# Performance work log

Measured on AMD Instinct MI355X. Metric: run time of the kernel, lower is better.

The kernel has to match this reference:

```python
import jax, jax.numpy as jnp
import numpy as np

B, L, D, H, FD, NL, NV, NN, MAXSPD = 2, 1024, 1024, 16, 512, 4, 5000, 5000, 30
DF = 4 * D
S = L + 2  # 1 graph token + 1 sos token + L data tokens
DH = D // H
NEG = -1e9  # finite stand-in for -inf query mask (constant per softmax row -> same probs, no NaNs)


def rmsnorm(x, w, eps=1e-6):
    return x * jax.lax.rsqrt(jnp.mean(x * x, axis=-1, keepdims=True) + eps) * w


def setup_inputs() -> dict:
    key = jax.random.key(0)
    ks = jax.random.split(key, 24)
    f = lambda k, sh, s=0.02: (jax.random.normal(k, sh, jnp.float32) * s)
    return {
        "graph_features": jax.random.normal(ks[0], (B, 1, D), jnp.float32),
        "input_features": jax.random.normal(ks[1], (B, L, FD), jnp.float32),
        "proj_W": f(ks[2], (FD, D)),
        "proj_b": jnp.zeros((D,), jnp.float32),
        "sos_token": f(ks[3], (1, 1, D)),
        "node_emb": f(ks[4], (NN, D)),
        "type_emb": f(ks[5], (2, D)),
        "pos_emb": f(ks[6], (S, D)),
        "spd_emb": f(ks[7], (MAXSPD + 2, H)),
        "attn_norm_w": jnp.ones((NL, D), jnp.float32),
        "wq": f(ks[8], (NL, D, D)),
        "wk": f(ks[9], (NL, D, D)),
        "wv": f(ks[10], (NL, D, D)),
        "wo": f(ks[11], (NL, D, D)),
        "ffn_norm_w": jnp.ones((NL, D), jnp.float32),
        "w1": f(ks[12], (NL, D, DF)),
        "w2": f(ks[13], (NL, DF, D)),
        "w3": f(ks[14], (NL, D, DF)),
        "final_norm_w": jnp.ones((D,), jnp.float32),
        "out_W": f(ks[15], (D, NV)),
        "out_b": jnp.zeros((NV,), jnp.float32),
        "subnode_ids": jax.random.randint(ks[16], (B, L), 0, NN),
        "token_mask_len": jax.random.randint(ks[17], (B,), 1, L),
        "spd_indices": jax.random.randint(ks[18], (B, L, L), 0, MAXSPD + 1),
        "start_pos": 0,
    }


def reference(graph_features, input_features, proj_W, proj_b, sos_token, node_emb,
              type_emb, pos_emb, spd_emb, attn_norm_w, wq, wk, wv, wo, ffn_norm_w,
              w1, w2, w3, final_norm_w, out_W, out_b,
              subnode_ids, token_mask_len, spd_indices, start_pos):
    bsz = input_features.shape[0]
    glen = graph_features.shape[1]  # 1

    # token embedding fusion
    h_data = input_features @ proj_W + proj_b                      # [B,L,D]
    sos = jnp.broadcast_to(sos_token, (bsz, 1, D))
    h_tokens = jnp.concatenate([sos, h_data], axis=1)              # [B,L+1,D]
    sub_ext = jnp.concatenate([jnp.zeros((bsz, 1), subnode_ids.dtype), subnode_ids], axis=1)
    h_tokens = h_tokens + node_emb[sub_ext] + type_emb[0]
    h_graph = graph_features + type_emb[1]
    h = jnp.concatenate([h_graph, h_tokens], axis=1)               # [B,S,D]
    seqlen = h.shape[1]

    # SPD relative bias -> [B,H,S,S]
    max_spd = spd_emb.shape[0] - 2
    full_spd = jnp.full((bsz, seqlen, seqlen), max_spd + 1, dtype=jnp.int32)
    full_spd = full_spd.at[:, 2:, 2:].set(spd_indices.astype(jnp.int32))
    full_spd = full_spd.at[:, 0, 0].set(0).at[:, 1, 1].set(0)
    graph_bias = jnp.transpose(spd_emb[full_spd], (0, 3, 1, 2))

    h = h + pos_emb[:seqlen]

    # additive query-validity mask [B,1,S,1] broadcast over keys
    positions = jnp.arange(seqlen)[None, :]
    valid = positions < (token_mask_len[:, None] + 1 + glen)
    mask = jnp.where(valid, 0.0, NEG).astype(h.dtype)[:, None, :, None]

    scale = 1.0 / np.sqrt(DH)
    n_heads = graph_bias.shape[1]
    for i in range(wq.shape[0]):
        x = rmsnorm(h, attn_norm_w[i])
        q = (x @ wq[i]).reshape(bsz, seqlen, n_heads, DH)
        k = (x @ wk[i]).reshape(bsz, seqlen, n_heads, DH)
        v = (x @ wv[i]).reshape(bsz, seqlen, n_heads, DH)
        scores = jnp.einsum('bqhd,bkhd->bhqk', q, k) * scale + graph_bias + mask
        p = jax.nn.softmax(scores, axis=-1)
        att = jnp.einsum('bhqk,bkhd->bqhd', p, v).reshape(bsz, seqlen, D) @ wo[i]
        h = h + att
        x2 = rmsnorm(h, ffn_norm_w[i])
        h = h + (jax.nn.silu(x2 @ w1[i]) * (x2 @ w3[i])) @ w2[i]

    h = rmsnorm(h, final_norm_w)
    h_seq = h[:, glen:, :]                                          # [B,L+1,D]
    return (h_seq @ out_W + out_b).astype(jnp.float32)
```

## Files before the change

kernel.cpp:

```cpp
#include <hip/hip_runtime.h>

#define DMODEL 1024
#define DFF    4096
#define NHEAD  16
#define DHEAD  64
#define LTOK   1024
#define SEQ    1026
#define SPAD   1088
#define MPAD   2176
#define NVOC   5000
#define NVOCP  5120
#define MOUT   2050

typedef float  floatx4 __attribute__((ext_vector_type(4)));
typedef __bf16 bf16x8  __attribute__((ext_vector_type(8)));

__device__ __forceinline__ unsigned short f2b(float f) {
  unsigned int u = __builtin_bit_cast(unsigned int, f);
  u += 0x7FFFu + ((u >> 16) & 1u);
  return (unsigned short)(u >> 16);
}
__device__ __forceinline__ float b2f(unsigned short v) {
  return __builtin_bit_cast(float, ((unsigned int)v) << 16);
}
__device__ __forceinline__ void gl2lds16(const void* g, void* l) {
  __builtin_amdgcn_global_load_lds((const __attribute__((address_space(1))) void*)g,
                                   (__attribute__((address_space(3))) void*)l, 16, 0, 0);
}
__device__ __forceinline__ floatx4 mfma16(bf16x8 a, bf16x8 b, floatx4 c) {
  return __builtin_amdgcn_mfma_f32_16x16x32_bf16(a, b, c, 0, 0, 0);
}

__global__ __launch_bounds__(256) void f2b_kernel(const float* __restrict__ s,
                                                  unsigned short* __restrict__ d, int n) {
  int i = (blockIdx.x * 256 + threadIdx.x) * 4;
  if (i >= n) return;
  float4 v = *(const float4*)(s + i);
  ushort4 o; o.x = f2b(v.x); o.y = f2b(v.y); o.z = f2b(v.z); o.w = f2b(v.w);
  *(ushort4*)(d + i) = o;
}

__global__ __launch_bounds__(256) void transconv_kernel(
    const float* __restrict__ p0, const float* __restrict__ p1,
    const float* __restrict__ p2, const float* __restrict__ p3,
    unsigned short* __restrict__ dst, long dstZ, int R, int C) {
  const float* src = (blockIdx.z == 0) ? p0 : (blockIdx.z == 1) ? p1 : (blockIdx.z == 2) ? p2 : p3;
  dst += dstZ * blockIdx.z;
  __shared__ float T[64][68];
  const int r0 = blockIdx.y * 64, c0 = blockIdx.x * 64;
  const int tr = threadIdx.x >> 4, tc = threadIdx.x & 15;
#pragma unroll
  for (int it = 0; it < 4; it++) {
    int rl = tr + it * 16;
    int cg = c0 + tc * 4;
    float4 v = {0.f, 0.f, 0.f, 0.f};
    if (cg < C) v = *(const float4*)(src + (size_t)(r0 + rl) * C + cg);
    T[rl][tc * 4 + 0] = v.x; T[rl][tc * 4 + 1] = v.y;
    T[rl][tc * 4 + 2] = v.z; T[rl][tc * 4 + 3] = v.w;
  }
  __syncthreads();
#pragma unroll
  for (int it = 0; it < 4; it++) {
    int ol = tr + it * 16;
    int oc = c0 + ol;
    if (oc < C) {
      ushort4 o;
      o.x = f2b(T[tc * 4 + 0][ol]); o.y = f2b(T[tc * 4 + 1][ol]);
      o.z = f2b(T[tc * 4 + 2][ol]); o.w = f2b(T[tc * 4 + 3][ol]);
      *(ushort4*)(dst + (size_t)oc * R + r0 + tc * 4) = o;
    }
  }
}

__global__ __launch_bounds__(256) void build_h_kernel(
    float* __restrict__ h, const float* __restrict__ gf, const float* __restrict__ sos,
    const float* __restrict__ nodeE, const float* __restrict__ typeE,
    const float* __restrict__ posE, const int* __restrict__ sub) {
  const int s = blockIdx.x, b = blockIdx.y;
  const int c = threadIdx.x * 4;
  float* o = h + ((size_t)(b * SPAD + s)) * DMODEL + c;
  if (s >= SEQ) { o[0] = 0.f; o[1] = 0.f; o[2] = 0.f; o[3] = 0.f; return; }
  float4 p = *(const float4*)(posE + (size_t)s * DMODEL + c);
  if (s == 0) {
    float4 g = *(const float4*)(gf + (size_t)b * DMODEL + c);
    float4 t = *(const float4*)(typeE + DMODEL + c);
    o[0] = g.x + t.x + p.x; o[1] = g.y + t.y + p.y;
    o[2] = g.z + t.z + p.z; o[3] = g.w + t.w + p.w;
  } else {
    float4 t = *(const float4*)(typeE + c);
    int nid = (s == 1) ? 0 : sub[b * LTOK + s - 2];
    float4 ne = *(const float4*)(nodeE + (size_t)nid * DMODEL + c);
    if (s == 1) {
      float4 ss = *(const float4*)(sos + c);
      o[0] = ss.x + ne.x + t.x + p.x; o[1] = ss.y + ne.y + t.y + p.y;
      o[2] = ss.z + ne.z + t.z + p.z; o[3] = ss.w + ne.w + t.w + p.w;
    } else {
      o[0] += ne.x + t.x + p.x; o[1] += ne.y + t.y + p.y;
      o[2] += ne.z + t.z + p.z; o[3] += ne.w + t.w + p.w;
    }
  }
}

__global__ __launch_bounds__(256) void rmsnorm_kernel(const float* __restrict__ h,
                                                      const float* __restrict__ w,
                                                      unsigned short* __restrict__ out,
                                                      int final_mode) {
  const int r = blockIdx.x;
  int srow = r;
  if (final_mode) {
    if (r >= MOUT) {
      ushort4 z = {0, 0, 0, 0};
      *(ushort4*)(out + (size_t)r * DMODEL + threadIdx.x * 4) = z;
      return;
    }
    int b = r / 1025;
    srow = b * SPAD + 1 + (r - b * 1025);
  }
  float4 x = *(const float4*)(h + (size_t)srow * DMODEL + threadIdx.x * 4);
  float ss = x.x * x.x + x.y * x.y + x.z * x.z + x.w * x.w;
#pragma unroll
  for (int off = 32; off > 0; off >>= 1) ss += __shfl_down(ss, off);
  __shared__ float red[4];
  if ((threadIdx.x & 63) == 0) red[threadIdx.x >> 6] = ss;
  __syncthreads();
  float rs = rsqrtf((red[0] + red[1] + red[2] + red[3]) * (1.f / 1024.f) + 1e-6f);
  float4 ww = *(const float4*)(w + threadIdx.x * 4);
  ushort4 o;
  o.x = f2b(x.x * rs * ww.x); o.y = f2b(x.y * rs * ww.y);
  o.z = f2b(x.z * rs * ww.z); o.w = f2b(x.w * rs * ww.w);
  *(ushort4*)(out + (size_t)r * DMODEL + threadIdx.x * 4) = o;
}

__global__ __launch_bounds__(320) void bidx_kernel(const int* __restrict__ spd,
                                                   unsigned char* __restrict__ bidx) {
  const int qg = blockIdx.x, b = blockIdx.y;
  const int i0 = threadIdx.x * 4;
  if (i0 >= SPAD) return;
  const int g = i0 >> 6, c = (i0 >> 2) & 15;
  unsigned char v[4];
#pragma unroll
  for (int n = 0; n < 4; n++) {
    int kg = g * 64 + n * 16 + c;
    unsigned char vv;
    if (qg >= SEQ || kg >= SEQ) {
      vv = 32;
    } else if (qg >= 2 && kg >= 2) {
      int idx = spd[((size_t)b * LTOK + (qg - 2)) * LTOK + (kg - 2)];
      vv = (unsigned char)(idx < 0 ? 0 : (idx > 31 ? 31 : idx));
    } else {
      vv = (qg == kg) ? 0 : 31;
    }
    v[n] = vv;
  }
  uchar4 o; o.x = v[0]; o.y = v[1]; o.z = v[2]; o.w = v[3];
  *(uchar4*)(bidx + ((size_t)b * SPAD + qg) * SPAD + i0) = o;
}

__global__ __launch_bounds__(256) void vtrans_kernel(const unsigned short* __restrict__ v,
                                                     unsigned short* __restrict__ vt) {
  const int st = blockIdx.x, hh = blockIdx.y, b = blockIdx.z;
  __shared__ unsigned short T[64][72];
  const int tr = threadIdx.x >> 4, tc = threadIdx.x & 15;
#pragma unroll
  for (int it = 0; it < 4; it++) {
    int r = tr + it * 16;
    ushort4 val = *(const ushort4*)(v + ((size_t)(b * SPAD + st * 64 + r)) * DMODEL + hh * DHEAD + tc * 4);
    T[r][tc * 4 + 0] = val.x; T[r][tc * 4 + 1] = val.y;
    T[r][tc * 4 + 2] = val.z; T[r][tc * 4 + 3] = val.w;
  }
  __syncthreads();
#pragma unroll
  for (int it = 0; it < 4; it++) {
    int d = tr + it * 16;
    ushort4 o;
    o.x = T[tc * 4 + 0][d]; o.y = T[tc * 4 + 1][d];
    o.z = T[tc * 4 + 2][d]; o.w = T[tc * 4 + 3][d];
    *(ushort4*)(vt + (((size_t)(b * NHEAD + hh)) * DHEAD + d) * SPAD + st * 64 + tc * 4) = o;
  }
}

#define PST 80
__global__ __launch_bounds__(512) void attn_kernel(
    const unsigned short* __restrict__ qb, const unsigned short* __restrict__ kb,
    const unsigned short* __restrict__ vt, unsigned short* __restrict__ attb,
    const float* __restrict__ spdE, const unsigned char* __restrict__ bidx,
    const int* __restrict__ tml) {
  const int hb = blockIdx.x;
  const int qt = blockIdx.y;
  const int hh = hb >> 1, bb = hb & 1;
  const int tid = threadIdx.x;
  const int w = tid >> 6, lane = tid & 63;
  const int quad = lane >> 4, l16 = lane & 15;

  __shared__ unsigned short Qs[128 * PST];
  __shared__ unsigned short Ks[64 * PST];
  __shared__ unsigned short Vts[64 * PST];
  __shared__ unsigned short Ps[8 * 16 * PST];
  __shared__ unsigned char Is[128 * 64];
  __shared__ float bias_tab[33];

  if (tid < 33) bias_tab[tid] = (tid < 32) ? spdE[tid * NHEAD + hh] : -3.0e38f;

#pragma unroll
  for (int jj = 0; jj < 2; jj++) {
    int c = tid + (jj << 9);
    int r = c >> 3, ch = c & 7;
    int qrow = qt * 128 + r; qrow = qrow < SPAD ? qrow : SPAD - 1;
    int4 val = *(const int4*)(qb + ((size_t)(bb * SPAD + qrow)) * DMODEL + hh * DHEAD + ch * 8);
    *(int4*)(Qs + r * PST + ch * 8) = val;
  }
  const int tmlb = tml[bb];

  const int sr = tid >> 3, sch = tid & 7;
  const int ir = tid >> 2, ic = (tid & 3) * 16;
  const int irow = min(qt * 128 + ir, SPAD - 1);
  int4 kreg, vreg, ireg;
  kreg = *(const int4*)(kb + ((size_t)(bb * SPAD + sr)) * DMODEL + hh * DHEAD + sch * 8);
  vreg = *(const int4*)(vt + (((size_t)(bb * NHEAD + hh)) * DHEAD + sr) * SPAD + sch * 8);
  ireg = *(const int4*)(bidx + ((size_t)bb * SPAD + irow) * SPAD + ic);
  __syncthreads();

  bf16x8 aq[2];
  aq[0] = *(const bf16x8*)(Qs + (w * 16 + l16) * PST + quad * 8);
  aq[1] = *(const bf16x8*)(Qs + (w * 16 + l16) * PST + 32 + quad * 8);

  floatx4 O[4];
  float m_i[4], l_i[4];
#pragma unroll
  for (int d = 0; d < 4; d++) { floatx4 z = {0.f, 0.f, 0.f, 0.f}; O[d] = z; }
#pragma unroll
  for (int r = 0; r < 4; r++) { m_i[r] = -3.0e38f; l_i[r] = 0.f; }

  unsigned short* PsW = Ps + w * 16 * PST;
  float maskv[4];
#pragma unroll
  for (int r = 0; r < 4; r++) {
    int qg = qt * 128 + w * 16 + quad * 4 + r;
    maskv[r] = (qg < tmlb + 2) ? 0.f : -1.0e9f;
  }

  for (int kt = 0; kt < 17; kt++) {
    *(int4*)(Ks + sr * PST + sch * 8) = kreg;
    *(int4*)(Vts + sr * PST + sch * 8) = vreg;
    *(int4*)(Is + ir * 64 + ic) = ireg;
    __syncthreads();

    if (kt < 16) {
      const int kn = kt + 1;
      kreg = *(const int4*)(kb + ((size_t)(bb * SPAD + kn * 64 + sr)) * DMODEL + hh * DHEAD + sch * 8);
      vreg = *(const int4*)(vt + (((size_t)(bb * NHEAD + hh)) * DHEAD + sr) * SPAD + kn * 64 + sch * 8);
      ireg = *(const int4*)(bidx + ((size_t)bb * SPAD + irow) * SPAD + kn * 64 + ic);
    }

    float sc[4][4];
#pragma unroll
    for (int ns = 0; ns < 4; ns++) {
      bf16x8 bk0 = *(const bf16x8*)(Ks + (ns * 16 + l16) * PST + quad * 8);
      bf16x8 bk1 = *(const bf16x8*)(Ks + (ns * 16 + l16) * PST + 32 + quad * 8);
      floatx4 c4 = {0.f, 0.f, 0.f, 0.f};
      c4 = mfma16(aq[0], bk0, c4);
      c4 = mfma16(aq[1], bk1, c4);
#pragma unroll
      for (int r = 0; r < 4; r++) sc[ns][r] = c4[r];
    }

#pragma unroll
    for (int r = 0; r < 4; r++) {
      int row = w * 16 + quad * 4 + r;
      unsigned int iw = *(const unsigned int*)(Is + row * 64 + l16 * 4);
#pragma unroll
      for (int ns = 0; ns < 4; ns++) {
        int idx = (iw >> (8 * ns)) & 0xff;
        sc[ns][r] = sc[ns][r] * 0.125f + bias_tab[idx] + maskv[r];
      }
    }

    float alpha[4];
#pragma unroll
    for (int r = 0; r < 4; r++) {
      float mx = fmaxf(fmaxf(sc[0][r], sc[1][r]), fmaxf(sc[2][r], sc[3][r]));
#pragma unroll
      for (int off = 1; off < 16; off <<= 1) mx = fmaxf(mx, __shfl_xor(mx, off));
      float mn = fmaxf(m_i[r], mx);
      alpha[r] = __expf(m_i[r] - mn);
      m_i[r] = mn;
      float rs = 0.f;
#pragma unroll
      for (int ns = 0; ns < 4; ns++) { float p = __expf(sc[ns][r] - mn); sc[ns][r] = p; rs += p; }
#pragma unroll
      for (int off = 1; off < 16; off <<= 1) rs += __shfl_xor(rs, off);
      l_i[r] = l_i[r] * alpha[r] + rs;
    }

#pragma unroll
    for (int ns = 0; ns < 4; ns++)
#pragma unroll
      for (int r = 0; r < 4; r++)
        PsW[(quad * 4 + r) * PST + ns * 16 + l16] = f2b(sc[ns][r]);

#pragma unroll
    for (int d = 0; d < 4; d++)
#pragma unroll
      for (int r = 0; r < 4; r++) O[d][r] *= alpha[r];

    bf16x8 ap0 = *(const bf16x8*)(PsW + l16 * PST + quad * 8);
    bf16x8 ap1 = *(const bf16x8*)(PsW + l16 * PST + 32 + quad * 8);
#pragma unroll
    for (int d = 0; d < 4; d++) {
      bf16x8 bv0 = *(const bf16x8*)(Vts + (d * 16 + l16) * PST + quad * 8);
      bf16x8 bv1 = *(const bf16x8*)(Vts + (d * 16 + l16) * PST + 32 + quad * 8);
      O[d] = mfma16(ap0, bv0, O[d]);
      O[d] = mfma16(ap1, bv1, O[d]);
    }
    __syncthreads();
  }

#pragma unroll
  for (int r = 0; r < 4; r++) {
    int qg = qt * 128 + w * 16 + quad * 4 + r;
    if (qg < SPAD) {
      float inv = 1.0f / l_i[r];
#pragma unroll
      for (int d = 0; d < 4; d++)
        attb[((size_t)(bb * SPAD + qg)) * DMODEL + hh * DHEAD + d * 16 + l16] = f2b(O[d][r] * inv);
    }
  }
}

__global__ __launch_bounds__(256) void silumul_kernel(const unsigned short* __restrict__ u,
                                                      unsigned short* __restrict__ g, int n) {
  int i = (blockIdx.x * 256 + threadIdx.x) * 4;
  if (i >= n) return;
  const unsigned short* u3 = u + n;
  ushort4 a = *(const ushort4*)(u + i);
  ushort4 c = *(const ushort4*)(u3 + i);
  ushort4 o;
  float x, y;
  x = b2f(a.x); y = b2f(c.x); o.x = f2b(x / (1.f + __expf(-x)) * y);
  x = b2f(a.y); y = b2f(c.y); o.y = f2b(x / (1.f + __expf(-x)) * y);
  x = b2f(a.z); y = b2f(c.z); o.z = f2b(x / (1.f + __expf(-x)) * y);
  x = b2f(a.w); y = b2f(c.w); o.w = f2b(x / (1.f + __expf(-x)) * y);
  *(ushort4*)(g + i) = o;
}

enum { EPI_BF16 = 0, EPI_RESID = 1, EPI_PROJ = 2, EPI_OUT = 3, EPI_ATOMIC = 4 };

template <int EPI>
__global__ __launch_bounds__(256) void gemm_bt_kernel(
    const unsigned short* __restrict__ A, const unsigned short* __restrict__ Bt,
    void* __restrict__ Cv, const float* __restrict__ bias,
    int M, int N, int K, int ld, long zA, long zB, long zC, int Mreal, int Nreal) {
  A += zA * blockIdx.z;
  Bt += zB * blockIdx.z;
  char* Cb = (char*)Cv + zC * blockIdx.z;

  const int tid = threadIdx.x;
  const int lane = tid & 63, wave = tid >> 6;
  const int quad = lane >> 4, l16 = lane & 15;
  const int wr = wave >> 1, wc = wave & 1;
  const int m0 = blockIdx.y << 7, n0 = blockIdx.x << 7;

  __shared__ unsigned short As[128 * 32];
  __shared__ unsigned short Bs[128 * 32];

  floatx4 acc[4][4];
  {
    floatx4 z = {0.f, 0.f, 0.f, 0.f};
#pragma unroll
    for (int i = 0; i < 4; i++)
#pragma unroll
      for (int j = 0; j < 4; j++) acc[i][j] = z;
  }

  for (int k0 = 0; k0 < K; k0 += 32) {
#pragma unroll
    for (int jj = 0; jj < 2; jj++) {
      int c = tid + (jj << 8);
      int r = c >> 2, kc = c & 3;
      gl2lds16(A + (size_t)(m0 + r) * ld + k0 + kc * 8, As + c * 8);
      gl2lds16(Bt + (size_t)(n0 + r) * ld + k0 + kc * 8, Bs + c * 8);
    }
    __syncthreads();
    bf16x8 a[4], b[4];
#pragma unroll
    for (int i = 0; i < 4; i++) a[i] = *(const bf16x8*)(As + (wr * 64 + i * 16 + l16) * 32 + quad * 8);
#pragma unroll
    for (int j = 0; j < 4; j++) b[j] = *(const bf16x8*)(Bs + (wc * 64 + j * 16 + l16) * 32 + quad * 8);
#pragma unroll
    for (int i = 0; i < 4; i++)
#pragma unroll
      for (int j = 0; j < 4; j++) acc[i][j] = mfma16(a[i], b[j], acc[i][j]);
    __syncthreads();
  }

#pragma unroll
  for (int i = 0; i < 4; i++) {
    const int rb = m0 + wr * 64 + i * 16 + quad * 4;
#pragma unroll
    for (int j = 0; j < 4; j++) {
      const int col = n0 + wc * 64 + j * 16 + l16;
#pragma unroll
      for (int r = 0; r < 4; r++) {
        const int row = rb + r;
        float v = acc[i][j][r];
        if constexpr (EPI == EPI_BF16) {
          ((unsigned short*)Cb)[(size_t)row * N + col] = f2b(v);
        } else if constexpr (EPI == EPI_RESID) {
          float* C = (float*)Cb;
          C[(size_t)row * N + col] += v;
        } else if constexpr (EPI == EPI_PROJ) {
          float* C = (float*)Cb;
          int rr = (row >> 10) * SPAD + 2 + (row & 1023);
          C[(size_t)rr * N + col] = v + bias[col];
        } else if constexpr (EPI == EPI_ATOMIC) {
          atomicAdd(&((float*)Cb)[(size_t)row * N + col], v);
        } else {
          if (row < Mreal && col < Nreal)
            ((float*)Cb)[(size_t)row * Nreal + col] = v + bias[col];
        }
      }
    }
  }
}

extern "C" void kernel_launch(void* const* d_in, const int* in_sizes, int n_in,
                              void* d_out, int out_size, void* d_ws, size_t ws_size,
                              hipStream_t stream) {
  const float* gf    = (const float*)d_in[0];
  const float* inpf  = (const float*)d_in[1];
  const float* projW = (const float*)d_in[2];
  const float* projB = (const float*)d_in[3];
  const float* sos   = (const float*)d_in[4];
  const float* nodeE = (const float*)d_in[5];
  const float* typeE = (const float*)d_in[6];
  const float* posE  = (const float*)d_in[7];
  const float* spdE  = (const float*)d_in[8];
  const float* attnW = (const float*)d_in[9];
  const float* wq    = (const float*)d_in[10];
  const float* wk    = (const float*)d_in[11];
  const float* wv    = (const float*)d_in[12];
  const float* wo    = (const float*)d_in[13];
  const float* ffnW  = (const float*)d_in[14];
  const float* w1    = (const float*)d_in[15];
  const float* w2    = (const float*)d_in[16];
  const float* w3    = (const float*)d_in[17];
  const float* finW  = (const float*)d_in[18];
  const float* outW  = (const float*)d_in[19];
  const float* outB  = (const float*)d_in[20];
  const int*   sub   = (const int*)d_in[21];
  const int*   tml   = (const int*)d_in[22];
  const int*   spd   = (const int*)d_in[23];
  float* out = (float*)d_out;
  (void)in_sizes; (void)n_in; (void)out_size; (void)ws_size;

  char* ws = (char*)d_ws;
  constexpr size_t OFF_H     = 0;
  constexpr size_t OFF_XB    = 8912896;
  constexpr size_t OFF_Q     = 13369344;
  constexpr size_t OFF_K     = 17825792;
  constexpr size_t OFF_V     = 22282240;
  constexpr size_t OFF_VT    = 26738688;
  constexpr size_t OFF_ATT   = 31195136;
  constexpr size_t OFF_U     = 35651584;
  constexpr size_t OFF_G     = 71303168;
  constexpr size_t OFF_XF    = 89128960;
  constexpr size_t OFF_INB   = 93585408;
  constexpr size_t OFF_PROJT = 95682560;
  constexpr size_t OFF_OUTWT = 96731136;
  constexpr size_t OFF_SLAB  = 107216896;

  float*          h    = (float*)(ws + OFF_H);
  unsigned short* xb   = (unsigned short*)(ws + OFF_XB);
  unsigned short* qbuf = (unsigned short*)(ws + OFF_Q);
  unsigned short* kbuf = (unsigned short*)(ws + OFF_K);
  unsigned short* vbuf = (unsigned short*)(ws + OFF_V);
  unsigned short* vtb  = (unsigned short*)(ws + OFF_VT);
  unsigned short* attb = (unsigned short*)(ws + OFF_ATT);
  unsigned short* ubuf = (unsigned short*)(ws + OFF_U);
  unsigned short* gbuf = (unsigned short*)(ws + OFF_G);
  unsigned short* xf   = (unsigned short*)(ws + OFF_XF);
  unsigned char*  bidx = (unsigned char*)(ws + OFF_XF);
  unsigned short* inb  = (unsigned short*)(ws + OFF_INB);
  unsigned short* projT = (unsigned short*)(ws + OFF_PROJT);
  unsigned short* outWT = (unsigned short*)(ws + OFF_OUTWT);
  unsigned short* slab  = (unsigned short*)(ws + OFF_SLAB);

  const long DD = (long)DMODEL * DMODEL;
  const long DDF = (long)DMODEL * DFF;
  const long ZC_TOK = (long)MPAD * DMODEL * 2;
  const long ZC_FF  = (long)MPAD * DFF * 2;

  f2b_kernel<<<1024, 256, 0, stream>>>(inpf, inb, 2048 * 512);
  transconv_kernel<<<dim3(16, 8, 1), 256, 0, stream>>>(projW, projW, projW, projW, projT, 0, 512, 1024);
  transconv_kernel<<<dim3(79, 16, 1), 256, 0, stream>>>(outW, outW, outW, outW, outWT, 0, 1024, NVOC);
  bidx_kernel<<<dim3(SPAD, 2), 320, 0, stream>>>(spd, bidx);

  gemm_bt_kernel<EPI_PROJ><<<dim3(8, 16, 1), 256, 0, stream>>>(
      inb, projT, h, projB, 2048, 1024, 512, 512, 0, 0, 0, 0, 0);
  build_h_kernel<<<dim3(SPAD, 2), 256, 0, stream>>>(h, gf, sos, nodeE, typeE, posE, sub);

  for (int i = 0; i < 4; i++) {
    transconv_kernel<<<dim3(16, 16, 4), 256, 0, stream>>>(
        wq + (long)i * DD, wk + (long)i * DD, wv + (long)i * DD, wo + (long)i * DD,
        slab, DD, 1024, 1024);
    transconv_kernel<<<dim3(64, 16, 2), 256, 0, stream>>>(
        w1 + (long)i * DDF, w3 + (long)i * DDF, w1, w1,
        slab + 4 * DD, DDF, 1024, 4096);
    transconv_kernel<<<dim3(16, 64, 1), 256, 0, stream>>>(
        w2 + (long)i * DDF, w2, w2, w2,
        slab + 12 * DD, 0, 4096, 1024);

    rmsnorm_kernel<<<MPAD, 256, 0, stream>>>(h, attnW + i * DMODEL, xb, 0);
    gemm_bt_kernel<EPI_BF16><<<dim3(8, 17, 3), 256, 0, stream>>>(
        xb, slab, qbuf, nullptr, MPAD, 1024, 1024, 1024, 0, DD, ZC_TOK, 0, 0);
    vtrans_kernel<<<dim3(17, 16, 2), 256, 0, stream>>>(vbuf, vtb);
    attn_kernel<<<dim3(32, 9, 1), 512, 0, stream>>>(qbuf, kbuf, vtb, attb, spdE, bidx, tml);
    gemm_bt_kernel<EPI_ATOMIC><<<dim3(8, 17, 2), 256, 0, stream>>>(
        attb, slab + 3 * DD, h, nullptr, MPAD, 1024, 512, 1024, 512, 512, 0, 0, 0);

    rmsnorm_kernel<<<MPAD, 256, 0, stream>>>(h, ffnW + i * DMODEL, xb, 0);
    gemm_bt_kernel<EPI_BF16><<<dim3(32, 17, 2), 256, 0, stream>>>(
        xb, slab + 4 * DD, ubuf, nullptr, MPAD, 4096, 1024, 1024, 0, DDF, ZC_FF, 0, 0);
    silumul_kernel<<<8704, 256, 0, stream>>>(ubuf, gbuf, MPAD * DFF);
    gemm_bt_kernel<EPI_ATOMIC><<<dim3(8, 17, 4), 256, 0, stream>>>(
        gbuf, slab + 12 * DD, h, nullptr, MPAD, 1024, 1024, 4096, 1024, 1024, 0, 0, 0);
  }

  rmsnorm_kernel<<<MPAD, 256, 0, stream>>>(h, finW, xf, 1);
  gemm_bt_kernel<EPI_OUT><<<dim3(40, 17, 1), 256, 0, stream>>>(
      xf, outWT, out, outB, MPAD, NVOCP, 1024, 1024, 0, 0, 0, MOUT, NVOC);
}
```

Measured before the change: 1.466 ms.

## Fuse FFN w1/w3 GEMMs with SiLU-mul and deepen GEMM K-tile with swizzled LDS

Replaces the batched w1/w3 GEMM plus separate silumul pass with one kernel that computes both projections per tile and applies SiLU(u1)*u3 in the epilogue. This removes the round trip of the large intermediate U buffer and one launch per layer. The generic GEMM also moves from a K-step of 32 to 64 with an XOR-swizzled LDS layout to cut bank conflicts and halve the number of barriers. The fused kernel holds two accumulator sets and three 16 KB LDS tiles, which raises register and LDS pressure and may lower occupancy.

```diff
diff --git a/kernel.cpp b/kernel.cpp
--- a/kernel.cpp
+++ b/kernel.cpp
@@ -327,20 +327,77 @@
   }
 }
 
-__global__ __launch_bounds__(256) void silumul_kernel(const unsigned short* __restrict__ u,
-                                                      unsigned short* __restrict__ g, int n) {
-  int i = (blockIdx.x * 256 + threadIdx.x) * 4;
-  if (i >= n) return;
-  const unsigned short* u3 = u + n;
-  ushort4 a = *(const ushort4*)(u + i);
-  ushort4 c = *(const ushort4*)(u3 + i);
-  ushort4 o;
-  float x, y;
-  x = b2f(a.x); y = b2f(c.x); o.x = f2b(x / (1.f + __expf(-x)) * y);
-  x = b2f(a.y); y = b2f(c.y); o.y = f2b(x / (1.f + __expf(-x)) * y);
-  x = b2f(a.z); y = b2f(c.z); o.z = f2b(x / (1.f + __expf(-x)) * y);
-  x = b2f(a.w); y = b2f(c.w); o.w = f2b(x / (1.f + __expf(-x)) * y);
-  *(ushort4*)(g + i) = o;
+__global__ __launch_bounds__(256) void ffn13_kernel(
+    const unsigned short* __restrict__ A, const unsigned short* __restrict__ B1,
+    const unsigned short* __restrict__ B3, unsigned short* __restrict__ G) {
+  const int tid = threadIdx.x;
+  const int lane = tid & 63, wave = tid >> 6;
+  const int quad = lane >> 4, l16 = lane & 15;
+  const int wr = wave >> 1, wc = wave & 1;
+  const int m0 = blockIdx.y << 7, n0 = blockIdx.x << 7;
+
+  __shared__ unsigned short As[128 * 64];
+  __shared__ unsigned short B1s[128 * 64];
+  __shared__ unsigned short B3s[128 * 64];
+
+  floatx4 acc1[4][4], acc3[4][4];
+  {
+    floatx4 z = {0.f, 0.f, 0.f, 0.f};
+#pragma unroll
+    for (int i = 0; i < 4; i++)
+#pragma unroll
+      for (int j = 0; j < 4; j++) { acc1[i][j] = z; acc3[i][j] = z; }
+  }
+
+  const int kcs8 = (((tid & 7) ^ ((tid >> 3) & 7))) * 8;
+  const int lsw = l16 & 7;
+
+  for (int k0 = 0; k0 < 1024; k0 += 64) {
+#pragma unroll
+    for (int jj = 0; jj < 4; jj++) {
+      int c = tid + (jj << 8);
+      int r = c >> 3;
+      gl2lds16(A + (size_t)(m0 + r) * 1024 + k0 + kcs8, As + c * 8);
+      gl2lds16(B1 + (size_t)(n0 + r) * 1024 + k0 + kcs8, B1s + c * 8);
+      gl2lds16(B3 + (size_t)(n0 + r) * 1024 + k0 + kcs8, B3s + c * 8);
+    }
+    __syncthreads();
+#pragma unroll
+    for (int h = 0; h < 2; h++) {
+      const int ch = (((h << 2) + quad) ^ lsw) * 8;
+      bf16x8 a[4], b1[4], b3[4];
+#pragma unroll
+      for (int i = 0; i < 4; i++) a[i] = *(const bf16x8*)(As + (wr * 64 + i * 16 + l16) * 64 + ch);
+#pragma unroll
+      for (int j = 0; j < 4; j++) {
+        b1[j] = *(const bf16x8*)(B1s + (wc * 64 + j * 16 + l16) * 64 + ch);
+        b3[j] = *(const bf16x8*)(B3s + (wc * 64 + j * 16 + l16) * 64 + ch);
+      }
+#pragma unroll
+      for (int i = 0; i < 4; i++)
+#pragma unroll
+        for (int j = 0; j < 4; j++) {
+          acc1[i][j] = mfma16(a[i], b1[j], acc1[i][j]);
+          acc3[i][j] = mfma16(a[i], b3[j], acc3[i][j]);
+        }
+    }
+    __syncthreads();
+  }
+
+#pragma unroll
+  for (int i = 0; i < 4; i++) {
+    const int rb = m0 + wr * 64 + i * 16 + quad * 4;
+#pragma unroll
+    for (int j = 0; j < 4; j++) {
+      const int col = n0 + wc * 64 + j * 16 + l16;
+#pragma unroll
+      for (int r = 0; r < 4; r++) {
+        float u1 = acc1[i][j][r], u3 = acc3[i][j][r];
+        float g = u1 / (1.f + __expf(-u1)) * u3;
+        G[(size_t)(rb + r) * DFF + col] = f2b(g);
+      }
+    }
+  }
 }
 
 enum { EPI_BF16 = 0, EPI_RESID = 1, EPI_PROJ = 2, EPI_OUT = 3, EPI_ATOMIC = 4 };
@@ -360,8 +417,8 @@
   const int wr = wave >> 1, wc = wave & 1;
   const int m0 = blockIdx.y << 7, n0 = blockIdx.x << 7;
 
-  __shared__ unsigned short As[128 * 32];
-  __shared__ unsigned short Bs[128 * 32];
+  __shared__ unsigned short As[128 * 64];
+  __shared__ unsigned short Bs[128 * 64];
 
   floatx4 acc[4][4];
   {
@@ -372,24 +429,31 @@
       for (int j = 0; j < 4; j++) acc[i][j] = z;
   }
 
-  for (int k0 = 0; k0 < K; k0 += 32) {
-#pragma unroll
-    for (int jj = 0; jj < 2; jj++) {
+  const int kcs8 = (((tid & 7) ^ ((tid >> 3) & 7))) * 8;
+  const int lsw = l16 & 7;
+
+  for (int k0 = 0; k0 < K; k0 += 64) {
+#pragma unroll
+    for (int jj = 0; jj < 4; jj++) {
       int c = tid + (jj << 8);
-      int r = c >> 2, kc = c & 3;
-      gl2lds16(A + (size_t)(m0 + r) * ld + k0 + kc * 8, As + c * 8);
-      gl2lds16(Bt + (size_t)(n0 + r) * ld + k0 + kc * 8, Bs + c * 8);
+      int r = c >> 3;
+      gl2lds16(A + (size_t)(m0 + r) * ld + k0 + kcs8, As + c * 8);
+      gl2lds16(Bt + (size_t)(n0 + r) * ld + k0 + kcs8, Bs + c * 8);
     }
     __syncthreads();
-    bf16x8 a[4], b[4];
-#pragma unroll
-    for (int i = 0; i < 4; i++) a[i] = *(const bf16x8*)(As + (wr * 64 + i * 16 + l16) * 32 + quad * 8);
-#pragma unroll
-    for (int j = 0; j < 4; j++) b[j] = *(const bf16x8*)(Bs + (wc * 64 + j * 16 + l16) * 32 + quad * 8);
-#pragma unroll
-    for (int i = 0; i < 4; i++)
-#pragma unroll
-      for (int j = 0; j < 4; j++) acc[i][j] = mfma16(a[i], b[j], acc[i][j]);
+#pragma unroll
+    for (int h = 0; h < 2; h++) {
+      const int ch = (((h << 2) + quad) ^ lsw) * 8;
+      bf16x8 a[4], b[4];
+#pragma unroll
+      for (int i = 0; i < 4; i++) a[i] = *(const bf16x8*)(As + (wr * 64 + i * 16 + l16) * 64 + ch);
+#pragma unroll
+      for (int j = 0; j < 4; j++) b[j] = *(const bf16x8*)(Bs + (wc * 64 + j * 16 + l16) * 64 + ch);
+#pragma unroll
+      for (int i = 0; i < 4; i++)
+#pragma unroll
+        for (int j = 0; j < 4; j++) acc[i][j] = mfma16(a[i], b[j], acc[i][j]);
+    }
     __syncthreads();
   }
 
@@ -461,7 +525,6 @@
   constexpr size_t OFF_V     = 22282240;
   constexpr size_t OFF_VT    = 26738688;
   constexpr size_t OFF_ATT   = 31195136;
-  constexpr size_t OFF_U     = 35651584;
   constexpr size_t OFF_G     = 71303168;
   constexpr size_t OFF_XF    = 89128960;
   constexpr size_t OFF_INB   = 93585408;
@@ -476,7 +539,6 @@
   unsigned short* vbuf = (unsigned short*)(ws + OFF_V);
   unsigned short* vtb  = (unsigned short*)(ws + OFF_VT);
   unsigned short* attb = (unsigned short*)(ws + OFF_ATT);
-  unsigned short* ubuf = (unsigned short*)(ws + OFF_U);
   unsigned short* gbuf = (unsigned short*)(ws + OFF_G);
   unsigned short* xf   = (unsigned short*)(ws + OFF_XF);
   unsigned char*  bidx = (unsigned char*)(ws + OFF_XF);
@@ -488,7 +550,6 @@
   const long DD = (long)DMODEL * DMODEL;
   const long DDF = (long)DMODEL * DFF;
   const long ZC_TOK = (long)MPAD * DMODEL * 2;
-  const long ZC_FF  = (long)MPAD * DFF * 2;
 
   f2b_kernel<<<1024, 256, 0, stream>>>(inpf, inb, 2048 * 512);
   transconv_kernel<<<dim3(16, 8, 1), 256, 0, stream>>>(projW, projW, projW, projW, projT, 0, 512, 1024);
@@ -519,9 +580,7 @@
         attb, slab + 3 * DD, h, nullptr, MPAD, 1024, 512, 1024, 512, 512, 0, 0, 0);
 
     rmsnorm_kernel<<<MPAD, 256, 0, stream>>>(h, ffnW + i * DMODEL, xb, 0);
-    gemm_bt_kernel<EPI_BF16><<<dim3(32, 17, 2), 256, 0, stream>>>(
-        xb, slab + 4 * DD, ubuf, nullptr, MPAD, 4096, 1024, 1024, 0, DDF, ZC_FF, 0, 0);
-    silumul_kernel<<<8704, 256, 0, stream>>>(ubuf, gbuf, MPAD * DFF);
+    ffn13_kernel<<<dim3(32, 17, 1), 256, 0, stream>>>(xb, slab + 4 * DD, slab + 8 * DD, gbuf);
     gemm_bt_kernel<EPI_ATOMIC><<<dim3(8, 17, 4), 256, 0, stream>>>(
         gbuf, slab + 12 * DD, h, nullptr, MPAD, 1024, 1024, 4096, 1024, 1024, 0, 0, 0);
   }
```

Result: slower. 1.501 ms (+2.4%).
